# Kernel tuning notes

Measured on AMD Instinct MI355X. Metric: run time of the kernel, lower is better.

## Reference

```python
import jax, jax.numpy as jnp
import numpy as np

def setup_inputs() -> dict:
    key = jax.random.key(0)
    ks = jax.random.split(key, 8)
    b, n, dim = 2, 2048, 512
    h, d, K, M = 8, 64, 32, 131072
    x = jax.random.normal(ks[0], (b, n, dim), dtype=jnp.float32)
    mem_db = jax.random.normal(ks[1], (b, M, 2, d), dtype=jnp.float32)
    knn_idx = jax.random.randint(ks[2], (b, h, n, K), 0, M)
    mem_mask = jax.random.randint(ks[3], (b, h, n, K), 0, 2).astype(bool)
    Wq = jax.random.normal(ks[4], (h * d, dim), dtype=jnp.float32) * 0.02
    Wkv = jax.random.normal(ks[5], (2 * d, dim), dtype=jnp.float32) * 0.02
    Wout = jax.random.normal(ks[6], (dim, h * d), dtype=jnp.float32) * 0.02
    scale_param = jnp.ones((h, 1, 1), dtype=jnp.float32) * np.log(20.0)
    return {"x": x, "mem_db": mem_db, "knn_idx": knn_idx, "mem_mask": mem_mask,
            "Wq": Wq, "Wkv": Wkv, "Wout": Wout, "scale_param": scale_param}

def reference(x, mem_db, knn_idx, mem_mask, Wq, Wkv, Wout, scale_param):
    b, n, dim = x.shape
    h = scale_param.shape[0]
    d = Wq.shape[0] // h
    # projections
    q = jnp.einsum('bnc,ec->bne', x, Wq).reshape(b, n, h, d).transpose(0, 2, 1, 3)  # b h n d
    q = q / jnp.linalg.norm(q, axis=-1, keepdims=True).clip(1e-12)  # l2norm
    kv = jnp.einsum('bnc,ec->bne', x, Wkv)  # [b,n,2d]; detached + added to memory (side effect only)
    scale = jnp.exp(scale_param)  # [h,1,1]
    # per-query KNN gather: mem_db [b,M,2,d], knn_idx [b,h,n,K] -> [b,h,n,K,2,d]
    mem_kv = jax.vmap(lambda db, ix: db[ix])(mem_db, knn_idx)
    mem_k = mem_kv[..., 0, :]  # b h n K d
    mem_v = mem_kv[..., 1, :]
    sim = jnp.einsum('bhid,bhijd->bhij', q, mem_k) * scale  # b h n K
    mask_value = -jnp.finfo(sim.dtype).max
    sim = jnp.where(mem_mask, sim, mask_value)
    attn = jax.nn.softmax(sim, axis=-1)  # stable softmax
    out = jnp.einsum('bhij,bhijd->bhid', attn, mem_v)  # b h n d
    out = out.transpose(0, 2, 1, 3).reshape(b, n, h * d)
    return jnp.einsum('bne,ce->bnc', out, Wout)
```

## Files before the change

### kernel.cpp

```cpp
#include <hip/hip_runtime.h>
#include <hip/hip_bf16.h>
#include <math.h>

#define B_SZ 2
#define N_SEQ 2048
#define DIM 512
#define H_HEADS 8
#define D_HEAD 64
#define K_NN 32
#define M_DB 131072

typedef __attribute__((ext_vector_type(8))) short bf16x8;
typedef __attribute__((ext_vector_type(4))) float f32x4;

#define GLL16(g, l)                                                       \
    __builtin_amdgcn_global_load_lds(                                     \
        (const __attribute__((address_space(1))) unsigned int*)(g),       \
        (__attribute__((address_space(3))) unsigned int*)(l), 16, 0, 0)

__device__ __forceinline__ void cvt_hi_lo(float f, short& h, short& l) {
    unsigned u = __float_as_uint(f);
    unsigned uh = u + (0x7fffu + ((u >> 16) & 1u));
    h = (short)(uh >> 16);
    float r = f - __uint_as_float((uh >> 16) << 16);
    unsigned ur = __float_as_uint(r);
    l = (short)((ur + (0x7fffu + ((ur >> 16) & 1u))) >> 16);
}

__device__ __forceinline__ void split4(float4 a, ushort4& h, ushort4& l) {
    short hh, ll;
    cvt_hi_lo(a.x, hh, ll); h.x = hh; l.x = ll;
    cvt_hi_lo(a.y, hh, ll); h.y = hh; l.y = ll;
    cvt_hi_lo(a.z, hh, ll); h.z = hh; l.z = ll;
    cvt_hi_lo(a.w, hh, ll); h.w = hh; l.w = ll;
}

__global__ __launch_bounds__(256) void prep_kernel(
    const float4* __restrict__ x, const float4* __restrict__ wq,
    const float4* __restrict__ wout,
    ushort4* __restrict__ xhi, ushort4* __restrict__ xlo,
    ushort4* __restrict__ qhi, ushort4* __restrict__ qlo,
    ushort4* __restrict__ ohi, ushort4* __restrict__ olo,
    const unsigned char* __restrict__ mb, int* __restrict__ flag)
{
    const int bid = blockIdx.x;
    const int t = threadIdx.x;
    if (bid < 2048) {
        int i = bid * 256 + t;
        ushort4 h, l;
        split4(x[i], h, l);
        xhi[i] = h; xlo[i] = l;
    } else if (bid < 2560) {
        int i = (bid - 2048) * 256 + t;
        const int n4 = DIM * DIM / 4;
        const float4* src = (i < n4) ? wq : wout;
        ushort4* dh = (i < n4) ? qhi : ohi;
        ushort4* dl = (i < n4) ? qlo : olo;
        int j = (i < n4) ? i : i - n4;
        ushort4 h, l;
        split4(src[j], h, l);
        dh[j] = h; dl[j] = l;
    } else {
        if (t < 64) {
            unsigned char v = 0;
            for (int e = t; e < 1024; e += 64) {
                v |= mb[4 * e + 1];
                v |= mb[4 * e + 2];
                v |= mb[4 * e + 3];
            }
            unsigned long long any = __ballot(v != 0);
            if (t == 0) *flag = (any != 0ull) ? 1 : 0;
        }
    }
}

__global__ __launch_bounds__(256) void gemm_mfma_lds(
    const unsigned short* __restrict__ Ahi, const unsigned short* __restrict__ Alo,
    const unsigned short* __restrict__ Bhi, const unsigned short* __restrict__ Blo,
    float* __restrict__ C, int Mdim, int Ndim, int Kdim)
{
    __shared__ char lds[3][16384];
    const int t = threadIdx.x;
    const int w = t >> 6, lane = t & 63;
    const int r = lane & 15, qd = lane >> 4;
    const int wm = w & 1, wn = w >> 1;
    const int m0 = blockIdx.x * 64;
    const int n0 = blockIdx.y * 64;

    const unsigned short* gsrc[4];
#pragma unroll
    for (int j = 0; j < 4; ++j) {
        const int cl = j * 4 + w;
        const int isB = cl >> 3;
        const int c = cl & 7;
        const int p = c >> 2, h = c & 3;
        const int row = (isB ? n0 : m0) + 16 * h + r;
        const unsigned short* plane =
            isB ? (p ? Blo : Bhi) : (p ? Alo : Ahi);
        gsrc[j] = plane + (size_t)row * Kdim + 8 * qd;
    }

    f32x4 acc[2][2];
#pragma unroll
    for (int i = 0; i < 2; ++i)
#pragma unroll
        for (int j = 0; j < 2; ++j) acc[i][j] = (f32x4){0.f, 0.f, 0.f, 0.f};

    auto stage = [&](int buf, int kstep) {
#pragma unroll
        for (int j = 0; j < 4; ++j) {
            const int cl = j * 4 + w;
            GLL16(gsrc[j] + kstep * 32, &lds[buf][cl * 1024]);
        }
    };

    auto compute = [&](int buf) {
        const char* base = lds[buf];
        bf16x8 A8[2][2], B8[2][2];
#pragma unroll
        for (int p = 0; p < 2; ++p)
#pragma unroll
            for (int i = 0; i < 2; ++i) {
                A8[p][i] = *(const bf16x8*)(
                    base + (p * 4 + 2 * wm + i) * 1024 + lane * 16);
                B8[p][i] = *(const bf16x8*)(
                    base + 8192 + (p * 4 + 2 * wn + i) * 1024 + lane * 16);
            }
#pragma unroll
        for (int mi = 0; mi < 2; ++mi)
#pragma unroll
            for (int ni = 0; ni < 2; ++ni) {
                acc[mi][ni] = __builtin_amdgcn_mfma_f32_16x16x32_bf16(
                    A8[0][mi], B8[0][ni], acc[mi][ni], 0, 0, 0);
                acc[mi][ni] = __builtin_amdgcn_mfma_f32_16x16x32_bf16(
                    A8[0][mi], B8[1][ni], acc[mi][ni], 0, 0, 0);
                acc[mi][ni] = __builtin_amdgcn_mfma_f32_16x16x32_bf16(
                    A8[1][mi], B8[0][ni], acc[mi][ni], 0, 0, 0);
            }
    };

    const int nsteps = Kdim >> 5;
    stage(0, 0);
    stage(1, 1);
    int bc = 0;
    for (int ks = 0; ks < nsteps - 1; ++ks) {
        asm volatile("s_waitcnt vmcnt(4)" ::: "memory");
        __builtin_amdgcn_s_barrier();
        if (ks + 2 < nsteps) {
            int bs = bc + 2; if (bs >= 3) bs -= 3;
            stage(bs, ks + 2);
        }
        compute(bc);
        if (++bc == 3) bc = 0;
    }
    asm volatile("s_waitcnt vmcnt(0)" ::: "memory");
    __builtin_amdgcn_s_barrier();
    compute(bc);

#pragma unroll
    for (int mi = 0; mi < 2; ++mi)
#pragma unroll
        for (int ni = 0; ni < 2; ++ni)
#pragma unroll
            for (int rr = 0; rr < 4; ++rr)
                C[(size_t)(m0 + 32 * wm + 16 * mi + qd * 4 + rr) * Ndim +
                  n0 + 32 * wn + 16 * ni + r] = acc[mi][ni][rr];
}

__global__ __launch_bounds__(256) void attn_kernel(
    const float* __restrict__ qbuf,
    const float* __restrict__ mem_db,
    const int* __restrict__ knn_idx,
    const void* __restrict__ mem_mask,
    const float* __restrict__ scale_param,
    const int* __restrict__ flag,
    unsigned short* __restrict__ out_hi,
    unsigned short* __restrict__ out_lo)
{
    const int wave = blockIdx.x * 4 + (threadIdx.x >> 6);
    const int lane = threadIdx.x & 63;
    const int sub = lane & 15, grp = lane >> 4;
    const int i = wave % N_SEQ;
    const int bh = wave / N_SEQ;
    const int hi = bh % H_HEADS;
    const int bi = bh / H_HEADS;

    const int bytelayout = *flag;

    const size_t kb = ((size_t)(bi * H_HEADS + hi) * N_SEQ + i) * K_NN;
    int idxv = 0, maskv = 0;
    if (lane < K_NN) {
        idxv = knn_idx[kb + lane];
        if (bytelayout)
            maskv = ((const unsigned char*)mem_mask)[kb + lane] ? 1 : 0;
        else
            maskv = ((const int*)mem_mask)[kb + lane] ? 1 : 0;
    }

    const float* qrow = qbuf + (size_t)(bi * N_SEQ + i) * DIM + hi * D_HEAD;
    float qv = qrow[lane];
    float ss = qv * qv;
#pragma unroll
    for (int s = 32; s; s >>= 1) ss += __shfl_xor(ss, s);
    qv = qv / fmaxf(sqrtf(ss), 1e-12f);

    float q4[4];
#pragma unroll
    for (int c = 0; c < 4; ++c) q4[c] = __shfl(qv, 4 * sub + c);

    const float scale = __expf(scale_param[hi]);

    unsigned long long mbits = __ballot(maskv != 0);
    const bool allmasked = (mbits == 0ull);

    const float* dbb = mem_db + (size_t)bi * M_DB * (2 * D_HEAD);

    float4 kk[8], vv[8];
#pragma unroll
    for (int g = 0; g < 8; ++g) {
        int idx = __shfl(idxv, 4 * g + grp);
        bool mrow = (mbits >> (4 * g + grp)) & 1ull;
        size_t koff = mrow ? (size_t)idx * (2 * D_HEAD) : 0;
        size_t voff = (mrow || allmasked) ? (size_t)idx * (2 * D_HEAD) : 0;
        kk[g] = *(const float4*)(dbb + koff + 4 * sub);
        vv[g] = *(const float4*)(dbb + voff + D_HEAD + 4 * sub);
    }

    float s8[8];
#pragma unroll
    for (int g = 0; g < 8; ++g) {
        float p = q4[0] * kk[g].x + q4[1] * kk[g].y + q4[2] * kk[g].z + q4[3] * kk[g].w;
        p += __shfl_xor(p, 1);
        p += __shfl_xor(p, 2);
        p += __shfl_xor(p, 4);
        p += __shfl_xor(p, 8);
        s8[g] = p;
    }

    float simlane = -INFINITY;
#pragma unroll
    for (int g = 0; g < 8; ++g) {
        float tv = __shfl(s8[g], (lane & 3) << 4);
        if ((lane >> 2) == g) simlane = tv;
    }
    if (lane < K_NN)
        simlane = maskv ? simlane * scale : -3.402823466e38f;

    float m = simlane;
#pragma unroll
    for (int s = 32; s; s >>= 1) m = fmaxf(m, __shfl_xor(m, s));
    float w = __expf(simlane - m);
    float l = w;
#pragma unroll
    for (int s = 32; s; s >>= 1) l += __shfl_xor(l, s);
    float winv = w / l;

    float4 o = {0.f, 0.f, 0.f, 0.f};
#pragma unroll
    for (int g = 0; g < 8; ++g) {
        float wg = __shfl(winv, 4 * g + grp);
        o.x = fmaf(wg, vv[g].x, o.x);
        o.y = fmaf(wg, vv[g].y, o.y);
        o.z = fmaf(wg, vv[g].z, o.z);
        o.w = fmaf(wg, vv[g].w, o.w);
    }
#pragma unroll
    for (int s = 16; s <= 32; s <<= 1) {
        o.x += __shfl_xor(o.x, s);
        o.y += __shfl_xor(o.y, s);
        o.z += __shfl_xor(o.z, s);
        o.w += __shfl_xor(o.w, s);
    }
    if (grp == 0) {
        ushort4 h, l4;
        split4(o, h, l4);
        size_t off = ((size_t)(bi * N_SEQ + i) * DIM + hi * D_HEAD + 4 * sub) >> 2;
        ((ushort4*)out_hi)[off] = h;
        ((ushort4*)out_lo)[off] = l4;
    }
}

extern "C" void kernel_launch(void* const* d_in, const int* in_sizes, int n_in,
                              void* d_out, int out_size, void* d_ws, size_t ws_size,
                              hipStream_t stream) {
    const float* x        = (const float*)d_in[0];
    const float* mem_db   = (const float*)d_in[1];
    const int*   knn_idx  = (const int*)d_in[2];
    const void*  mem_mask = d_in[3];
    const float* Wq       = (const float*)d_in[4];
    const float* Wout     = (const float*)d_in[6];
    const float* scale_p  = (const float*)d_in[7];
    float* out = (float*)d_out;

    const int Mrows = B_SZ * N_SEQ;
    const int n_x   = Mrows * DIM;
    const int n_w   = DIM * DIM;

    char* ws = (char*)d_ws;
    int* flag = (int*)ws;
    float* qbuf = (float*)(ws + 256);
    unsigned short* x_hi  = (unsigned short*)(qbuf + (size_t)n_x);
    unsigned short* x_lo  = x_hi + n_x;
    unsigned short* ao_hi = x_lo + n_x;
    unsigned short* ao_lo = ao_hi + n_x;
    unsigned short* wq_hi = ao_lo + n_x;
    unsigned short* wq_lo = wq_hi + n_w;
    unsigned short* wo_hi = wq_lo + n_w;
    unsigned short* wo_lo = wo_hi + n_w;

    prep_kernel<<<2561, 256, 0, stream>>>(
        (const float4*)x, (const float4*)Wq, (const float4*)Wout,
        (ushort4*)x_hi, (ushort4*)x_lo,
        (ushort4*)wq_hi, (ushort4*)wq_lo, (ushort4*)wo_hi, (ushort4*)wo_lo,
        (const unsigned char*)mem_mask, flag);

    dim3 ggrid(Mrows / 64, DIM / 64);
    gemm_mfma_lds<<<ggrid, 256, 0, stream>>>(x_hi, x_lo, wq_hi, wq_lo, qbuf,
                                             Mrows, DIM, DIM);

    const int n_waves = B_SZ * H_HEADS * N_SEQ;
    attn_kernel<<<n_waves / 4, 256, 0, stream>>>(qbuf, mem_db, knn_idx, mem_mask,
                                                 scale_p, flag, ao_hi, ao_lo);

    gemm_mfma_lds<<<ggrid, 256, 0, stream>>>(ao_hi, ao_lo, wo_hi, wo_lo, out,
                                             Mrows, DIM, DIM);
}
```

Baseline: 261.1 us.

## Load GEMM B operand directly into registers, stage only A via LDS

The split-bf16 GEMM now stages only the A hi/lo tiles through LDS with global_load_lds. The B hi/lo fragments are read straight from global memory into double-buffered registers, one k-step ahead. The main loop is unrolled by two to alternate the register buffers, and the vmcnt wait is adjusted to match. This halves LDS per block, which may raise occupancy, but B loads now bypass LDS reuse and go through the cache per wave. The loop tail also issues redundant clamped loads.

```diff
diff --git a/kernel.cpp b/kernel.cpp
--- a/kernel.cpp
+++ b/kernel.cpp
@@ -79,7 +79,7 @@
     const unsigned short* __restrict__ Bhi, const unsigned short* __restrict__ Blo,
     float* __restrict__ C, int Mdim, int Ndim, int Kdim)
 {
-    __shared__ char lds[3][16384];
+    __shared__ char lds[3][8192];
     const int t = threadIdx.x;
     const int w = t >> 6, lane = t & 63;
     const int r = lane & 15, qd = lane >> 4;
@@ -87,18 +87,22 @@
     const int m0 = blockIdx.x * 64;
     const int n0 = blockIdx.y * 64;
 
-    const unsigned short* gsrc[4];
-#pragma unroll
-    for (int j = 0; j < 4; ++j) {
-        const int cl = j * 4 + w;
-        const int isB = cl >> 3;
-        const int c = cl & 7;
-        const int p = c >> 2, h = c & 3;
-        const int row = (isB ? n0 : m0) + 16 * h + r;
-        const unsigned short* plane =
-            isB ? (p ? Blo : Bhi) : (p ? Alo : Ahi);
-        gsrc[j] = plane + (size_t)row * Kdim + 8 * qd;
-    }
+    const unsigned short* gA0;
+    const unsigned short* gA1;
+    {
+        const int row = m0 + 16 * w + r;
+        gA0 = Ahi + (size_t)row * Kdim + 8 * qd;
+        gA1 = Alo + (size_t)row * Kdim + 8 * qd;
+    }
+
+    const unsigned short* gB[2][2];
+#pragma unroll
+    for (int p = 0; p < 2; ++p)
+#pragma unroll
+        for (int ni = 0; ni < 2; ++ni) {
+            const int row = n0 + 32 * wn + 16 * ni + r;
+            gB[p][ni] = (p ? Blo : Bhi) + (size_t)row * Kdim + 8 * qd;
+        }
 
     f32x4 acc[2][2];
 #pragma unroll
@@ -107,25 +111,27 @@
         for (int j = 0; j < 2; ++j) acc[i][j] = (f32x4){0.f, 0.f, 0.f, 0.f};
 
     auto stage = [&](int buf, int kstep) {
-#pragma unroll
-        for (int j = 0; j < 4; ++j) {
-            const int cl = j * 4 + w;
-            GLL16(gsrc[j] + kstep * 32, &lds[buf][cl * 1024]);
-        }
+        GLL16(gA0 + kstep * 32, &lds[buf][w * 1024]);
+        GLL16(gA1 + kstep * 32, &lds[buf][(w + 4) * 1024]);
     };
 
-    auto compute = [&](int buf) {
+    auto loadB = [&](bf16x8 (&B)[2][2], int kstep) {
+#pragma unroll
+        for (int p = 0; p < 2; ++p)
+#pragma unroll
+            for (int ni = 0; ni < 2; ++ni)
+                B[p][ni] = *(const bf16x8*)(gB[p][ni] + kstep * 32);
+    };
+
+    auto compute = [&](int buf, const bf16x8 (&B8)[2][2]) {
         const char* base = lds[buf];
-        bf16x8 A8[2][2], B8[2][2];
+        bf16x8 A8[2][2];
 #pragma unroll
         for (int p = 0; p < 2; ++p)
 #pragma unroll
-            for (int i = 0; i < 2; ++i) {
+            for (int i = 0; i < 2; ++i)
                 A8[p][i] = *(const bf16x8*)(
                     base + (p * 4 + 2 * wm + i) * 1024 + lane * 16);
-                B8[p][i] = *(const bf16x8*)(
-                    base + 8192 + (p * 4 + 2 * wn + i) * 1024 + lane * 16);
-            }
 #pragma unroll
         for (int mi = 0; mi < 2; ++mi)
 #pragma unroll
@@ -140,22 +146,32 @@
     };
 
     const int nsteps = Kdim >> 5;
+    bf16x8 Ba[2][2], Bb[2][2];
+    loadB(Ba, 0);
     stage(0, 0);
     stage(1, 1);
     int bc = 0;
-    for (int ks = 0; ks < nsteps - 1; ++ks) {
-        asm volatile("s_waitcnt vmcnt(4)" ::: "memory");
+    for (int it = 0; it < nsteps / 2; ++it) {
+        const int ks0 = 2 * it, ks1 = 2 * it + 1;
+        asm volatile("s_waitcnt vmcnt(2)" ::: "memory");
         __builtin_amdgcn_s_barrier();
-        if (ks + 2 < nsteps) {
+        loadB(Bb, ks0 + 1 < nsteps ? ks0 + 1 : nsteps - 1);
+        {
             int bs = bc + 2; if (bs >= 3) bs -= 3;
-            stage(bs, ks + 2);
+            stage(bs, ks0 + 2 < nsteps ? ks0 + 2 : nsteps - 1);
         }
-        compute(bc);
+        compute(bc, Ba);
         if (++bc == 3) bc = 0;
-    }
-    asm volatile("s_waitcnt vmcnt(0)" ::: "memory");
-    __builtin_amdgcn_s_barrier();
-    compute(bc);
+        asm volatile("s_waitcnt vmcnt(2)" ::: "memory");
+        __builtin_amdgcn_s_barrier();
+        loadB(Ba, ks1 + 1 < nsteps ? ks1 + 1 : nsteps - 1);
+        {
+            int bs = bc + 2; if (bs >= 3) bs -= 3;
+            stage(bs, ks1 + 2 < nsteps ? ks1 + 2 : nsteps - 1);
+        }
+        compute(bc, Bb);
+        if (++bc == 3) bc = 0;
+    }
 
 #pragma unroll
     for (int mi = 0; mi < 2; ++mi)
```

Result: slower. 275.4 us (+5.5%).
